# Optimization experiments

Measured on AMD Instinct MI355X. Metric: run time of the kernel, lower is better.

The kernel has to match this reference:

```python
import jax, jax.numpy as jnp
import numpy as np
import math

DIM = 2048
B, Q_LEN, KV_LEN = 8, 128, 4096


def setup_inputs() -> dict:
    key = jax.random.key(0)
    ks = jax.random.split(key, 8)
    x = jax.random.normal(ks[0], (B, Q_LEN, DIM), dtype=jnp.float32)
    mask = jnp.zeros((B, Q_LEN, KV_LEN + Q_LEN), dtype=bool)  # unused by the original forward
    k_cache = jax.random.normal(ks[1], (B, KV_LEN, DIM), dtype=jnp.float32)
    v_cache = jax.random.normal(ks[2], (B, KV_LEN, DIM), dtype=jnp.float32)
    scale = 1.0 / math.sqrt(DIM)
    wq = jax.random.normal(ks[3], (DIM, DIM), dtype=jnp.float32) * scale
    wk = jax.random.normal(ks[4], (DIM, DIM), dtype=jnp.float32) * scale
    wv = jax.random.normal(ks[5], (DIM, DIM), dtype=jnp.float32) * scale
    wo = jax.random.normal(ks[6], (DIM, DIM), dtype=jnp.float32) * scale
    return {"x": x, "mask": mask, "k_cache": k_cache, "v_cache": v_cache,
            "wq": wq, "wk": wk, "wv": wv, "wo": wo}


def reference(x, mask, k_cache, v_cache, wq, wk, wv, wo):
    # Linear layers (torch: y = x @ W^T)
    q = jnp.einsum('bsd,ed->bse', x, wq)
    k_new = jnp.einsum('bsd,ed->bse', x, wk)
    v_new = jnp.einsum('bsd,ed->bse', x, wv)
    # KV-cache growth via concat (the pattern the kernel replaces)
    k = jnp.concatenate([k_cache, k_new], axis=1)  # [B, KV+Q, D]
    v = jnp.concatenate([v_cache, v_new], axis=1)
    scale = 1.0 / math.sqrt(q.shape[-1])
    scores = jnp.einsum('bqd,bkd->bqk', q, k) * scale  # [B, Q, KV+Q]
    attn = jax.nn.softmax(scores, axis=-1)             # NOTE: mask is unused, as in original
    out = jnp.einsum('bqk,bkd->bqd', attn, v)
    return jnp.einsum('bqd,ed->bqe', out, wo)
```

## Files before the change

kernel.cpp:

```cpp
#include <hip/hip_runtime.h>

typedef __bf16 bf16;
typedef __bf16 bf16x4 __attribute__((ext_vector_type(4)));
typedef __bf16 bf16x8 __attribute__((ext_vector_type(8)));
typedef float f32x4 __attribute__((ext_vector_type(4)));

#define DIM   2048
#define BQ    128
#define KVL   4096
#define KVT   4224
#define SCALE 0.022097086912079608f

__device__ __forceinline__ int swz(int row, int col) {
  return row * 64 + (col ^ ((row & 7) << 3));
}

template<int R, int NTHR>
struct PBg {
  static constexpr int N8 = R * 64 / (NTHR * 8);
  bf16x8 v[N8];
  __device__ __forceinline__ void load(const bf16* __restrict__ src, int ld, int tid) {
    const int r0 = tid >> 3, c = (tid & 7) * 8;
    #pragma unroll
    for (int j = 0; j < N8; ++j)
      v[j] = *reinterpret_cast<const bf16x8*>(src + (size_t)(j * (NTHR / 8) + r0) * ld + c);
  }
  __device__ __forceinline__ void write(bf16* dst, int tid) {
    const int r0 = tid >> 3, c = (tid & 7) * 8;
    #pragma unroll
    for (int j = 0; j < N8; ++j)
      *reinterpret_cast<bf16x8*>(dst + swz(j * (NTHR / 8) + r0, c)) = v[j];
  }
};

struct PU64 {
  float4 v[4];
  int r0, c;
  __device__ __forceinline__ void init(int tid) { r0 = tid >> 4; c = (tid & 15) * 4; }
  __device__ __forceinline__ void loadF(const float* __restrict__ src, int ld) {
    #pragma unroll
    for (int j = 0; j < 4; ++j)
      v[j] = *reinterpret_cast<const float4*>(src + (size_t)(j * 16 + r0) * ld + c);
  }
  __device__ __forceinline__ void loadB(const bf16* __restrict__ src, int ld) {
    #pragma unroll
    for (int j = 0; j < 4; ++j) {
      bf16x4 t = *reinterpret_cast<const bf16x4*>(src + (size_t)(j * 16 + r0) * ld + c);
      v[j].x = (float)t[0]; v[j].y = (float)t[1]; v[j].z = (float)t[2]; v[j].w = (float)t[3];
    }
  }
  __device__ __forceinline__ void write(bf16* dst) {
    #pragma unroll
    for (int j = 0; j < 4; ++j) {
      bf16x4 b;
      b[0] = (bf16)v[j].x; b[1] = (bf16)v[j].y; b[2] = (bf16)v[j].z; b[3] = (bf16)v[j].w;
      *reinterpret_cast<bf16x4*>(dst + swz(j * 16 + r0, c)) = b;
    }
  }
};

struct PVT {
  float v[16];
  int vn, vk0;
  __device__ __forceinline__ void init(int tid) { vn = tid & 63; vk0 = (tid >> 6) * 16; }
  __device__ __forceinline__ void loadF(const float* __restrict__ src) {
    #pragma unroll
    for (int i = 0; i < 16; ++i) v[i] = src[(size_t)(vk0 + i) * DIM + vn];
  }
  __device__ __forceinline__ void loadB(const bf16* __restrict__ src) {
    #pragma unroll
    for (int i = 0; i < 16; ++i) v[i] = (float)src[(size_t)(vk0 + i) * DIM + vn];
  }
  __device__ __forceinline__ void write(bf16* dst) {
    #pragma unroll
    for (int j = 0; j < 4; ++j) {
      bf16x4 t;
      #pragma unroll
      for (int i = 0; i < 4; ++i) t[i] = (bf16)v[4 * j + i];
      *reinterpret_cast<bf16x4*>(dst + swz(vn, vk0 + 4 * j)) = t;
    }
  }
};

template<int MF, int NF>
__device__ __forceinline__ void mma_tile(const bf16* As, const bf16* Bs,
                                         f32x4 (&acc)[MF][NF], int l, int wm, int wn) {
  const int ar = l & 15;
  const int ak = (l >> 4) * 8;
  bf16x8 a[MF][2], b[NF][2];
  #pragma unroll
  for (int mi = 0; mi < MF; ++mi)
    #pragma unroll
    for (int kk = 0; kk < 2; ++kk)
      a[mi][kk] = *reinterpret_cast<const bf16x8*>(As + swz(wm + mi * 16 + ar, kk * 32 + ak));
  #pragma unroll
  for (int ni = 0; ni < NF; ++ni)
    #pragma unroll
    for (int kk = 0; kk < 2; ++kk)
      b[ni][kk] = *reinterpret_cast<const bf16x8*>(Bs + swz(wn + ni * 16 + ar, kk * 32 + ak));
  #pragma unroll
  for (int kk = 0; kk < 2; ++kk)
    #pragma unroll
    for (int mi = 0; mi < MF; ++mi)
      #pragma unroll
      for (int ni = 0; ni < NF; ++ni)
        acc[mi][ni] = __builtin_amdgcn_mfma_f32_16x16x32_bf16(
            a[mi][kk], b[ni][kk], acc[mi][ni], 0, 0, 0);
}

__global__ __launch_bounds__(256) void k_cvt(const float* __restrict__ x,
    const float* __restrict__ wq, const float* __restrict__ wk,
    const float* __restrict__ wv, const float* __restrict__ wo,
    bf16* __restrict__ xb, bf16* __restrict__ wb) {
  const int seg = blockIdx.y;
  const float* src; bf16* dst; int n; float sc = 1.0f;
  if (seg == 0)      { src = x;  dst = xb;            n = 1024 * DIM; }
  else if (seg == 1) { src = wq; dst = wb;            n = DIM * DIM; sc = SCALE; }
  else if (seg == 2) { src = wk; dst = wb + 1 * DIM * DIM; n = DIM * DIM; }
  else if (seg == 3) { src = wv; dst = wb + 2 * DIM * DIM; n = DIM * DIM; }
  else               { src = wo; dst = wb + 3 * DIM * DIM; n = DIM * DIM; }
  const int i0 = (blockIdx.x * 256 + threadIdx.x) * 8;
  if (i0 >= n) return;
  #pragma unroll
  for (int h = 0; h < 2; ++h) {
    float4 v = *reinterpret_cast<const float4*>(src + i0 + 4 * h);
    bf16x4 b;
    b[0] = (bf16)(v.x * sc); b[1] = (bf16)(v.y * sc);
    b[2] = (bf16)(v.z * sc); b[3] = (bf16)(v.w * sc);
    *reinterpret_cast<bf16x4*>(dst + i0 + 4 * h) = b;
  }
}

__global__ __launch_bounds__(128) void k_qkv(const bf16* __restrict__ xb,
    const bf16* __restrict__ wb,
    bf16* __restrict__ qb, bf16* __restrict__ kb, bf16* __restrict__ vb) {
  __shared__ bf16 As[128 * 64];
  __shared__ bf16 Bs[64 * 64];
  const int nt = blockIdx.x;
  const int w  = nt >> 5;
  const int col0 = (nt & 31) * 64;
  bf16* __restrict__ O = (w == 0) ? qb : (w == 1) ? kb : vb;
  const int m0 = blockIdx.y * 128;
  const int tid = threadIdx.x, l = tid & 63, wid = tid >> 6;
  const int wm = wid * 64;
  const bf16* Ap = xb + (size_t)m0 * DIM;
  const bf16* Bp = wb + (size_t)nt * 64 * DIM;
  PBg<128, 128> pa; PBg<64, 128> pb;
  f32x4 acc[4][4] = {};
  pa.load(Ap, DIM, tid); pb.load(Bp, DIM, tid);
  pa.write(As, tid);     pb.write(Bs, tid);
  __syncthreads();
  constexpr int NT = DIM / 64;
  for (int kt = 0; kt < NT; ++kt) {
    if (kt + 1 < NT) { pa.load(Ap + (kt + 1) * 64, DIM, tid); pb.load(Bp + (kt + 1) * 64, DIM, tid); }
    mma_tile<4, 4>(As, Bs, acc, l, wm, 0);
    __syncthreads();
    if (kt + 1 < NT) { pa.write(As, tid); pb.write(Bs, tid); }
    __syncthreads();
  }
  const int rr = (l >> 4) * 4, cc = l & 15;
  #pragma unroll
  for (int mi = 0; mi < 4; ++mi)
    #pragma unroll
    for (int ni = 0; ni < 4; ++ni)
      #pragma unroll
      for (int r = 0; r < 4; ++r)
        O[(size_t)(m0 + wm + mi * 16 + rr + r) * DIM + col0 + ni * 16 + cc] =
            (bf16)acc[mi][ni][r];
}

__global__ __launch_bounds__(256) void k_scores(const bf16* __restrict__ qb,
    const bf16* __restrict__ kb, const float* __restrict__ kcache,
    float* __restrict__ scores) {
  __shared__ bf16 As[2][128 * 64];
  __shared__ bf16 Bs[2][64 * 64];
  const int nt = blockIdx.x;
  const int b  = blockIdx.y;
  const int tid = threadIdx.x, l = tid & 63, wid = tid >> 6;
  const int wm = (wid >> 1) * 64, wn = (wid & 1) * 32;
  const bf16* Q = qb + (size_t)b * BQ * DIM;
  const bool useCache = (nt < 64);
  const float* Bf = kcache + ((size_t)b * KVL + nt * 64) * DIM;
  const bf16*  Bb = kb + ((size_t)b * BQ + (nt - 64) * 64) * DIM;
  PBg<128, 256> pa; PU64 pu; pu.init(tid);
  f32x4 acc[4][2] = {};
  pa.load(Q, DIM, tid);
  if (useCache) pu.loadF(Bf, DIM); else pu.loadB(Bb, DIM);
  pa.write(As[0], tid); pu.write(Bs[0]);
  int cur = 0;
  constexpr int NT = DIM / 64;
  for (int kt = 0; kt < NT; ++kt) {
    if (kt + 1 < NT) {
      pa.load(Q + (kt + 1) * 64, DIM, tid);
      if (useCache) pu.loadF(Bf + (kt + 1) * 64, DIM); else pu.loadB(Bb + (kt + 1) * 64, DIM);
    }
    __syncthreads();
    mma_tile<4, 2>(As[cur], Bs[cur], acc, l, wm, wn);
    if (kt + 1 < NT) { pa.write(As[cur ^ 1], tid); pu.write(Bs[cur ^ 1]); }
    cur ^= 1;
  }
  const int rr = (l >> 4) * 4, cc = l & 15;
  #pragma unroll
  for (int mi = 0; mi < 4; ++mi)
    #pragma unroll
    for (int ni = 0; ni < 2; ++ni)
      #pragma unroll
      for (int r = 0; r < 4; ++r)
        scores[((size_t)b * BQ + wm + mi * 16 + rr + r) * KVT + nt * 64 + wn + ni * 16 + cc] =
            acc[mi][ni][r];
}

__global__ __launch_bounds__(256) void k_softmax(const float* __restrict__ scores,
                                                 bf16* __restrict__ attn) {
  __shared__ float s[KVT];
  __shared__ float red[8];
  const int row = blockIdx.x;
  const int tid = threadIdx.x;
  const size_t base = (size_t)row * KVT;
  float lm = -1e30f;
  for (int i = tid; i < KVT; i += 256) {
    float v = scores[base + i];
    s[i] = v;
    lm = fmaxf(lm, v);
  }
  #pragma unroll
  for (int off = 32; off >= 1; off >>= 1) lm = fmaxf(lm, __shfl_xor(lm, off, 64));
  if ((tid & 63) == 0) red[tid >> 6] = lm;
  __syncthreads();
  const float m = fmaxf(fmaxf(red[0], red[1]), fmaxf(red[2], red[3]));
  float ls = 0.f;
  for (int i = tid; i < KVT; i += 256) {
    float e = __expf(s[i] - m);
    s[i] = e;
    ls += e;
  }
  #pragma unroll
  for (int off = 32; off >= 1; off >>= 1) ls += __shfl_xor(ls, off, 64);
  if ((tid & 63) == 0) red[4 + (tid >> 6)] = ls;
  __syncthreads();
  const float inv = 1.f / (red[4] + red[5] + red[6] + red[7]);
  for (int i = tid; i < KVT; i += 256) attn[base + i] = (bf16)(s[i] * inv);
}

__global__ __launch_bounds__(256) void k_pv(const bf16* __restrict__ attn,
    const float* __restrict__ vcache, const bf16* __restrict__ vb,
    float* __restrict__ pp) {
  __shared__ bf16 As[2][128 * 64];
  __shared__ bf16 VT[2][64 * 64];
  const int n0 = blockIdx.x * 64;
  const int b  = blockIdx.y;
  const int c  = blockIdx.z;
  const int tid = threadIdx.x, l = tid & 63, wid = tid >> 6;
  const int wm = (wid >> 1) * 64, wn = (wid & 1) * 32;
  const bf16* Ap = attn + (size_t)b * BQ * KVT + c * 2112;
  PBg<128, 256> pa; PVT pv; pv.init(tid);
  f32x4 acc[4][2] = {};
  auto loadV = [&](int lk) {
    const int grow = c * 2112 + lk * 64;
    if (grow < KVL) pv.loadF(vcache + ((size_t)b * KVL + grow) * DIM + n0);
    else            pv.loadB(vb + ((size_t)b * BQ + (grow - KVL)) * DIM + n0);
  };
  pa.load(Ap, KVT, tid); loadV(0);
  pa.write(As[0], tid);  pv.write(VT[0]);
  int cur = 0;
  constexpr int NT = 33;
  for (int kt = 0; kt < NT; ++kt) {
    if (kt + 1 < NT) { pa.load(Ap + (kt + 1) * 64, KVT, tid); loadV(kt + 1); }
    __syncthreads();
    mma_tile<4, 2>(As[cur], VT[cur], acc, l, wm, wn);
    if (kt + 1 < NT) { pa.write(As[cur ^ 1], tid); pv.write(VT[cur ^ 1]); }
    cur ^= 1;
  }
  float* P = pp + (size_t)c * 1024 * DIM;
  const int rr = (l >> 4) * 4, cc = l & 15;
  #pragma unroll
  for (int mi = 0; mi < 4; ++mi)
    #pragma unroll
    for (int ni = 0; ni < 2; ++ni)
      #pragma unroll
      for (int r = 0; r < 4; ++r)
        P[((size_t)b * BQ + wm + mi * 16 + rr + r) * DIM + n0 + wn + ni * 16 + cc] =
            acc[mi][ni][r];
}

__global__ __launch_bounds__(256) void k_pvcomb(const float* __restrict__ pp,
                                                bf16* __restrict__ ob) {
  const int i0 = (blockIdx.x * 256 + threadIdx.x) * 4;
  float4 a = *reinterpret_cast<const float4*>(pp + i0);
  float4 b = *reinterpret_cast<const float4*>(pp + 1024 * DIM + i0);
  bf16x4 o;
  o[0] = (bf16)(a.x + b.x); o[1] = (bf16)(a.y + b.y);
  o[2] = (bf16)(a.z + b.z); o[3] = (bf16)(a.w + b.w);
  *reinterpret_cast<bf16x4*>(ob + i0) = o;
}

__global__ __launch_bounds__(128) void k_oproj(const bf16* __restrict__ ob,
    const bf16* __restrict__ wob, float* __restrict__ po) {
  __shared__ bf16 As[128 * 64];
  __shared__ bf16 Bs[64 * 64];
  const int n0 = blockIdx.x * 64;
  const int m0 = blockIdx.y * 128;
  const int kz = blockIdx.z;
  const int tid = threadIdx.x, l = tid & 63, wid = tid >> 6;
  const int wm = wid * 64;
  const bf16* Ap = ob  + (size_t)m0 * DIM + kz * 1024;
  const bf16* Bp = wob + (size_t)n0 * DIM + kz * 1024;
  PBg<128, 128> pa; PBg<64, 128> pb;
  f32x4 acc[4][4] = {};
  pa.load(Ap, DIM, tid); pb.load(Bp, DIM, tid);
  pa.write(As, tid);     pb.write(Bs, tid);
  __syncthreads();
  constexpr int NT = 16;
  for (int kt = 0; kt < NT; ++kt) {
    if (kt + 1 < NT) { pa.load(Ap + (kt + 1) * 64, DIM, tid); pb.load(Bp + (kt + 1) * 64, DIM, tid); }
    mma_tile<4, 4>(As, Bs, acc, l, wm, 0);
    __syncthreads();
    if (kt + 1 < NT) { pa.write(As, tid); pb.write(Bs, tid); }
    __syncthreads();
  }
  float* P = po + (size_t)kz * 1024 * DIM;
  const int rr = (l >> 4) * 4, cc = l & 15;
  #pragma unroll
  for (int mi = 0; mi < 4; ++mi)
    #pragma unroll
    for (int ni = 0; ni < 4; ++ni)
      #pragma unroll
      for (int r = 0; r < 4; ++r)
        P[(size_t)(m0 + wm + mi * 16 + rr + r) * DIM + n0 + ni * 16 + cc] =
            acc[mi][ni][r];
}

__global__ __launch_bounds__(256) void k_ocomb(const float* __restrict__ po,
                                               float* __restrict__ out) {
  const int i0 = (blockIdx.x * 256 + threadIdx.x) * 4;
  float4 a = *reinterpret_cast<const float4*>(po + i0);
  float4 b = *reinterpret_cast<const float4*>(po + 1024 * DIM + i0);
  float4 o = {a.x + b.x, a.y + b.y, a.z + b.z, a.w + b.w};
  *reinterpret_cast<float4*>(out + i0) = o;
}

extern "C" void kernel_launch(void* const* d_in, const int* in_sizes, int n_in,
                              void* d_out, int out_size, void* d_ws, size_t ws_size,
                              hipStream_t stream) {
  const float* x      = (const float*)d_in[0];
  const float* kcache = (const float*)d_in[2];
  const float* vcache = (const float*)d_in[3];
  const float* wq     = (const float*)d_in[4];
  const float* wk     = (const float*)d_in[5];
  const float* wv     = (const float*)d_in[6];
  const float* wo     = (const float*)d_in[7];
  float* out = (float*)d_out;

  char* ws = (char*)d_ws;
  bf16*  xb     = (bf16*)(ws + 0);
  bf16*  wb     = (bf16*)(ws + 4194304);
  bf16*  qb     = (bf16*)(ws + 37748736);
  bf16*  kb     = (bf16*)(ws + 41943040);
  bf16*  vb     = (bf16*)(ws + 46137344);
  float* scores = (float*)(ws + 50331648);
  bf16*  attnb  = (bf16*)(ws + 67633152);
  bf16*  obuf   = (bf16*)(ws + 76283904);
  float* pp     = scores;
  bf16*  wob    = wb + (size_t)3 * DIM * DIM;

  k_cvt<<<dim3(2048, 5), 256, 0, stream>>>(x, wq, wk, wv, wo, xb, wb);
  k_qkv<<<dim3(96, 8), 128, 0, stream>>>(xb, wb, qb, kb, vb);
  k_scores<<<dim3(66, 8), 256, 0, stream>>>(qb, kb, kcache, scores);
  k_softmax<<<dim3(1024), 256, 0, stream>>>(scores, attnb);
  k_pv<<<dim3(32, 8, 2), 256, 0, stream>>>(attnb, vcache, vb, pp);
  k_pvcomb<<<dim3(2048), 256, 0, stream>>>(pp, obuf);
  k_oproj<<<dim3(32, 8, 2), 128, 0, stream>>>(obuf, wob, pp);
  k_ocomb<<<dim3(2048), 256, 0, stream>>>(pp, out);
}
```

Measured before the change: 257.5 us.

## Use direct global-to-LDS loads and 128x128 tiles in QKV and output projections

The QKV and output-projection GEMMs now stage A and B tiles through global_load_lds, which writes global memory straight into LDS with the XOR swizzle. This replaces the register round-trip and software prefetch. Block tiles grow from 128x64 to 128x128 with 256 threads, so each A tile is reused across more columns and the grid halves. The new loop no longer overlaps loads with MMA work (single-buffered load, sync, compute, sync), and the smaller grid lowers CU occupancy on these GEMMs.

```diff
diff --git a/kernel.cpp b/kernel.cpp
--- a/kernel.cpp
+++ b/kernel.cpp
@@ -13,6 +13,25 @@
 
 __device__ __forceinline__ int swz(int row, int col) {
   return row * 64 + (col ^ ((row & 7) << 3));
+}
+
+__device__ __forceinline__ void gload16(const bf16* g, bf16* l) {
+  __builtin_amdgcn_global_load_lds(
+      (const __attribute__((address_space(1))) void*)g,
+      (__attribute__((address_space(3))) void*)l, 16, 0, 0);
+}
+
+template<int R>
+__device__ __forceinline__ void gstage(const bf16* __restrict__ src, int ld,
+                                       bf16* dst, int wid, int lane) {
+  constexpr int OPS = R / 32;
+  const int rsub = lane >> 3;
+  const int schunk = (lane & 7) ^ rsub;
+  #pragma unroll
+  for (int j = 0; j < OPS; ++j) {
+    const int row0 = wid * (R / 4) + j * 8;
+    gload16(src + (size_t)(row0 + rsub) * ld + schunk * 8, dst + row0 * 64);
+  }
 }
 
 template<int R, int NTHR>
@@ -131,31 +150,27 @@
   }
 }
 
-__global__ __launch_bounds__(128) void k_qkv(const bf16* __restrict__ xb,
+__global__ __launch_bounds__(256) void k_qkv(const bf16* __restrict__ xb,
     const bf16* __restrict__ wb,
     bf16* __restrict__ qb, bf16* __restrict__ kb, bf16* __restrict__ vb) {
   __shared__ bf16 As[128 * 64];
-  __shared__ bf16 Bs[64 * 64];
+  __shared__ bf16 Bs[128 * 64];
   const int nt = blockIdx.x;
-  const int w  = nt >> 5;
-  const int col0 = (nt & 31) * 64;
+  const int w  = nt >> 4;
+  const int col0 = (nt & 15) * 128;
   bf16* __restrict__ O = (w == 0) ? qb : (w == 1) ? kb : vb;
   const int m0 = blockIdx.y * 128;
   const int tid = threadIdx.x, l = tid & 63, wid = tid >> 6;
-  const int wm = wid * 64;
+  const int wm = (wid >> 1) * 64, wn = (wid & 1) * 64;
   const bf16* Ap = xb + (size_t)m0 * DIM;
-  const bf16* Bp = wb + (size_t)nt * 64 * DIM;
-  PBg<128, 128> pa; PBg<64, 128> pb;
+  const bf16* Bp = wb + (size_t)nt * 128 * DIM;
   f32x4 acc[4][4] = {};
-  pa.load(Ap, DIM, tid); pb.load(Bp, DIM, tid);
-  pa.write(As, tid);     pb.write(Bs, tid);
-  __syncthreads();
   constexpr int NT = DIM / 64;
   for (int kt = 0; kt < NT; ++kt) {
-    if (kt + 1 < NT) { pa.load(Ap + (kt + 1) * 64, DIM, tid); pb.load(Bp + (kt + 1) * 64, DIM, tid); }
-    mma_tile<4, 4>(As, Bs, acc, l, wm, 0);
-    __syncthreads();
-    if (kt + 1 < NT) { pa.write(As, tid); pb.write(Bs, tid); }
+    gstage<128>(Ap + kt * 64, DIM, As, wid, l);
+    gstage<128>(Bp + kt * 64, DIM, Bs, wid, l);
+    __syncthreads();
+    mma_tile<4, 4>(As, Bs, acc, l, wm, wn);
     __syncthreads();
   }
   const int rr = (l >> 4) * 4, cc = l & 15;
@@ -165,7 +180,7 @@
     for (int ni = 0; ni < 4; ++ni)
       #pragma unroll
       for (int r = 0; r < 4; ++r)
-        O[(size_t)(m0 + wm + mi * 16 + rr + r) * DIM + col0 + ni * 16 + cc] =
+        O[(size_t)(m0 + wm + mi * 16 + rr + r) * DIM + col0 + wn + ni * 16 + cc] =
             (bf16)acc[mi][ni][r];
 }
 
@@ -294,28 +309,24 @@
   *reinterpret_cast<bf16x4*>(ob + i0) = o;
 }
 
-__global__ __launch_bounds__(128) void k_oproj(const bf16* __restrict__ ob,
+__global__ __launch_bounds__(256) void k_oproj(const bf16* __restrict__ ob,
     const bf16* __restrict__ wob, float* __restrict__ po) {
   __shared__ bf16 As[128 * 64];
-  __shared__ bf16 Bs[64 * 64];
-  const int n0 = blockIdx.x * 64;
+  __shared__ bf16 Bs[128 * 64];
+  const int n0 = blockIdx.x * 128;
   const int m0 = blockIdx.y * 128;
   const int kz = blockIdx.z;
   const int tid = threadIdx.x, l = tid & 63, wid = tid >> 6;
-  const int wm = wid * 64;
+  const int wm = (wid >> 1) * 64, wn = (wid & 1) * 64;
   const bf16* Ap = ob  + (size_t)m0 * DIM + kz * 1024;
   const bf16* Bp = wob + (size_t)n0 * DIM + kz * 1024;
-  PBg<128, 128> pa; PBg<64, 128> pb;
   f32x4 acc[4][4] = {};
-  pa.load(Ap, DIM, tid); pb.load(Bp, DIM, tid);
-  pa.write(As, tid);     pb.write(Bs, tid);
-  __syncthreads();
   constexpr int NT = 16;
   for (int kt = 0; kt < NT; ++kt) {
-    if (kt + 1 < NT) { pa.load(Ap + (kt + 1) * 64, DIM, tid); pb.load(Bp + (kt + 1) * 64, DIM, tid); }
-    mma_tile<4, 4>(As, Bs, acc, l, wm, 0);
-    __syncthreads();
-    if (kt + 1 < NT) { pa.write(As, tid); pb.write(Bs, tid); }
+    gstage<128>(Ap + kt * 64, DIM, As, wid, l);
+    gstage<128>(Bp + kt * 64, DIM, Bs, wid, l);
+    __syncthreads();
+    mma_tile<4, 4>(As, Bs, acc, l, wm, wn);
     __syncthreads();
   }
   float* P = po + (size_t)kz * 1024 * DIM;
@@ -326,7 +337,7 @@
     for (int ni = 0; ni < 4; ++ni)
       #pragma unroll
       for (int r = 0; r < 4; ++r)
-        P[(size_t)(m0 + wm + mi * 16 + rr + r) * DIM + n0 + ni * 16 + cc] =
+        P[(size_t)(m0 + wm + mi * 16 + rr + r) * DIM + n0 + wn + ni * 16 + cc] =
             acc[mi][ni][r];
 }
 
@@ -364,11 +375,11 @@
   bf16*  wob    = wb + (size_t)3 * DIM * DIM;
 
   k_cvt<<<dim3(2048, 5), 256, 0, stream>>>(x, wq, wk, wv, wo, xb, wb);
-  k_qkv<<<dim3(96, 8), 128, 0, stream>>>(xb, wb, qb, kb, vb);
+  k_qkv<<<dim3(48, 8), 256, 0, stream>>>(xb, wb, qb, kb, vb);
   k_scores<<<dim3(66, 8), 256, 0, stream>>>(qb, kb, kcache, scores);
   k_softmax<<<dim3(1024), 256, 0, stream>>>(scores, attnb);
   k_pv<<<dim3(32, 8, 2), 256, 0, stream>>>(attnb, vcache, vb, pp);
   k_pvcomb<<<dim3(2048), 256, 0, stream>>>(pp, obuf);
-  k_oproj<<<dim3(32, 8, 2), 128, 0, stream>>>(obuf, wob, pp);
+  k_oproj<<<dim3(16, 8, 2), 256, 0, stream>>>(obuf, wob, pp);
   k_ocomb<<<dim3(2048), 256, 0, stream>>>(pp, out);
 }
```

Measured after the change: 257.7 us. No clear change (+0.1%).
